# Kernel optimization log

Measured on AMD Instinct MI355X. Metric: run time of the kernel, lower is better.

## Reference

```python
import jax, jax.numpy as jnp
import numpy as np

H_MODEL = 1024
N_HEADS = 16
N_KV_HEADS = 4
HEAD_DIM = 64
SLIDING_WINDOW = 512
B, S = 2, 2048
NEG_INF = -1e9


def rotate_half(x):
    half = x.shape[-1] // 2
    return jnp.concatenate([-x[..., half:], x[..., :half]], axis=-1)


def setup_inputs() -> dict:
    key = jax.random.key(0)
    ks = jax.random.split(key, 8)
    hidden_states = jax.random.normal(ks[0], (B, S, H_MODEL), dtype=jnp.float32)
    # RoPE tables (HF style): cos/sin of shape [1, S, head_dim]
    inv_freq = 1.0 / (10000.0 ** (jnp.arange(0, HEAD_DIM, 2, dtype=jnp.float32) / HEAD_DIM))
    pos = jnp.arange(S, dtype=jnp.float32)
    freqs = jnp.einsum('s,d->sd', pos, inv_freq)            # [S, D/2]
    emb = jnp.concatenate([freqs, freqs], axis=-1)          # [S, D]
    cos = jnp.cos(emb)[None]                                # [1, S, D]
    sin = jnp.sin(emb)[None]
    # additive causal + sliding-window mask [1,1,S,S]
    i = jnp.arange(S)[:, None]
    j = jnp.arange(S)[None, :]
    allowed = (j <= i) & (i - j < SLIDING_WINDOW)
    attention_mask = jnp.where(allowed, 0.0, NEG_INF).astype(jnp.float32)[None, None]
    # projection weights (torch Linear stores [out, in]; y = x @ W.T)
    std = 0.02
    Wq = jax.random.normal(ks[1], (N_HEADS * HEAD_DIM, H_MODEL), dtype=jnp.float32) * std
    Wk = jax.random.normal(ks[2], (N_KV_HEADS * HEAD_DIM, H_MODEL), dtype=jnp.float32) * std
    Wv = jax.random.normal(ks[3], (N_KV_HEADS * HEAD_DIM, H_MODEL), dtype=jnp.float32) * std
    Wo = jax.random.normal(ks[4], (H_MODEL, N_HEADS * HEAD_DIM), dtype=jnp.float32) * std
    return {"hidden_states": hidden_states, "cos": cos, "sin": sin,
            "attention_mask": attention_mask, "Wq": Wq, "Wk": Wk, "Wv": Wv, "Wo": Wo}


def reference(hidden_states, cos, sin, attention_mask, Wq, Wk, Wv, Wo):
    b, s, _ = hidden_states.shape
    G = N_HEADS // N_KV_HEADS
    scaling = HEAD_DIM ** -0.5
    # QKV projections -> [B, H, S, D]
    q = jnp.einsum('bsh,oh->bso', hidden_states, Wq).reshape(b, s, N_HEADS, HEAD_DIM).transpose(0, 2, 1, 3)
    k = jnp.einsum('bsh,oh->bso', hidden_states, Wk).reshape(b, s, N_KV_HEADS, HEAD_DIM).transpose(0, 2, 1, 3)
    v = jnp.einsum('bsh,oh->bso', hidden_states, Wv).reshape(b, s, N_KV_HEADS, HEAD_DIM).transpose(0, 2, 1, 3)
    # RoPE (cos/sin broadcast over head dim via unsqueeze(1))
    c = cos[:, None, :, :]
    sn = sin[:, None, :, :]
    q = q * c + rotate_half(q) * sn
    k = k * c + rotate_half(k) * sn
    # GQA eager attention: group query heads over kv heads
    qg = q.reshape(b, N_KV_HEADS, G, s, HEAD_DIM)
    scores = jnp.einsum('bkgqd,bkpd->bkgqp', qg, k) * scaling  # [B,Hkv,G,S,S]
    scores = scores + attention_mask[:, :, None, :, :]
    probs = jax.nn.softmax(scores.astype(jnp.float32), axis=-1).astype(q.dtype)
    out = jnp.einsum('bkgqp,bkpd->bkgqd', probs, v)            # [B,Hkv,G,S,D]
    out = out.reshape(b, N_HEADS, s, HEAD_DIM).transpose(0, 2, 1, 3).reshape(b, s, N_HEADS * HEAD_DIM)
    return jnp.einsum('bso,ho->bsh', out, Wo)
```

## Files before the change

kernel.cpp:

```cpp
#include <hip/hip_runtime.h>
#include <hip/hip_bf16.h>

#define S_LEN 2048
#define NH 16
#define NKV 4
#define HD 64
#define WIN 512
#define BATCH 2

typedef __bf16 bf16_8 __attribute__((ext_vector_type(8)));
typedef float f32x4 __attribute__((ext_vector_type(4)));

__device__ inline bf16_8 cvt8(f32x4 a, f32x4 b) {
    bf16_8 r;
    r[0] = (__bf16)a[0]; r[1] = (__bf16)a[1]; r[2] = (__bf16)a[2]; r[3] = (__bf16)a[3];
    r[4] = (__bf16)b[0]; r[5] = (__bf16)b[1]; r[6] = (__bf16)b[2]; r[7] = (__bf16)b[3];
    return r;
}


__global__ __launch_bounds__(256) void cvt_pack(
    const float* __restrict__ hs, const float* __restrict__ Wq,
    const float* __restrict__ Wk, const float* __restrict__ Wv,
    const float* __restrict__ Wo,
    __bf16* __restrict__ hsp, __bf16* __restrict__ Wqp,
    __bf16* __restrict__ Wkp, __bf16* __restrict__ Wvp,
    __bf16* __restrict__ Wop)
{
    int i = blockIdx.x * 256 + threadIdx.x;
    const float* S; __bf16* P;
    if (i < 524288)      { S = hs; P = hsp; }
    else if (i < 655360) { S = Wq; P = Wqp; i -= 524288; }
    else if (i < 688128) { S = Wk; P = Wkp; i -= 655360; }
    else if (i < 720896) { S = Wv; P = Wvp; i -= 688128; }
    else                 { S = Wo; P = Wop; i -= 720896; }
    const int n = i >> 7;
    const int k = (i & 127) << 3;
    const f32x4 a = *(const f32x4*)(S + (size_t)n * 1024 + k);
    const f32x4 b = *(const f32x4*)(S + (size_t)n * 1024 + k + 4);
    const size_t dst = ((size_t)((n >> 4) * 32 + (k >> 5)) << 9)
                     + ((size_t)((n & 15) | (((k >> 3) & 3) << 4)) << 3);
    *(bf16_8*)(P + dst) = cvt8(a, b);
}

__device__ __forceinline__ void gemm_stream(
    const __bf16* __restrict__ Aq, const __bf16* __restrict__ Bq,
    f32x4 acc[2][4])
{
    const f32x4 fzero = {0.f, 0.f, 0.f, 0.f};
#pragma unroll
    for (int i = 0; i < 2; ++i)
#pragma unroll
        for (int nt = 0; nt < 4; ++nt) acc[i][nt] = fzero;

    bf16_8 b0[4], b1[4];
#pragma unroll
    for (int nt = 0; nt < 4; ++nt) {
        b0[nt] = *(const bf16_8*)(Bq + nt * 16384);
        b1[nt] = *(const bf16_8*)(Bq + nt * 16384 + 512);
    }

    for (int it = 0; it < 16; ++it) {
        bf16_8 a0[2], a1[2];
#pragma unroll
        for (int i = 0; i < 2; ++i) {
            a0[i] = *(const bf16_8*)(Aq + (size_t)(i * 32 + it * 2) * 512);
            a1[i] = *(const bf16_8*)(Aq + (size_t)(i * 32 + it * 2 + 1) * 512);
        }
        bf16_8 nb0[4], nb1[4];
        const bool pf = it < 15;
        if (pf) {
#pragma unroll
            for (int nt = 0; nt < 4; ++nt) {
                nb0[nt] = *(const bf16_8*)(Bq + nt * 16384 + (it + 1) * 1024);
                nb1[nt] = *(const bf16_8*)(Bq + nt * 16384 + (it + 1) * 1024 + 512);
            }
        }
#pragma unroll
        for (int i = 0; i < 2; ++i)
#pragma unroll
            for (int nt = 0; nt < 4; ++nt)
                acc[i][nt] = __builtin_amdgcn_mfma_f32_16x16x32_bf16(a0[i], b0[nt], acc[i][nt], 0, 0, 0);
#pragma unroll
        for (int i = 0; i < 2; ++i)
#pragma unroll
            for (int nt = 0; nt < 4; ++nt)
                acc[i][nt] = __builtin_amdgcn_mfma_f32_16x16x32_bf16(a1[i], b1[nt], acc[i][nt], 0, 0, 0);
        if (pf) {
#pragma unroll
            for (int nt = 0; nt < 4; ++nt) { b0[nt] = nb0[nt]; b1[nt] = nb1[nt]; }
        }
    }
}

__global__ __launch_bounds__(256, 4) void gemm_qkv(
    const __bf16* __restrict__ Apk,
    const __bf16* __restrict__ Wqp,
    const __bf16* __restrict__ Wkp,
    const __bf16* __restrict__ Wvp,
    __bf16* __restrict__ Qp,
    __bf16* __restrict__ Kf,
    __bf16* __restrict__ Vf,
    const float* __restrict__ cosb,
    const float* __restrict__ sinb)
{
    __shared__ __align__(16) __bf16 smem[9216];

    const int tid  = threadIdx.x;
    const int wave = tid >> 6;
    const int lane = tid & 63;
    const int wm   = wave & 1;
    const int wn   = wave >> 1;
    const int fm   = lane & 15;

    const int bx   = blockIdx.x;
    const int row0 = bx * 64;
    const int by   = blockIdx.y;

    const __bf16* Bp; int colb; int mode;
    if (by < 8)       { Bp = Wqp; colb = by * 128;        mode = 0; }
    else if (by < 10) { Bp = Wkp; colb = (by - 8) * 128;  mode = 1; }
    else              { Bp = Wvp; colb = (by - 10) * 128; mode = 2; }
    const int col0 = colb;

    const __bf16* Bq = Bp + (size_t)((colb + wn * 64) >> 4) * 16384 + (lane << 3);
    const __bf16* Aq = Apk + ((size_t)(bx * 4 + wm * 2) * 32) * 512 + (lane << 3);
    f32x4 acc[2][4];
    gemm_stream(Aq, Bq, acc);

    const int drow = (lane >> 4) << 2;
    const int cq   = col0 + wn * 64;
    const int bb   = row0 >> 11;
    const int sk0  = row0 & (S_LEN - 1);

    if (mode == 0) {
        const int lp = drow | ((fm >> 3) << 4);
#pragma unroll
        for (int i = 0; i < 2; ++i) {
            const size_t t1 = (size_t)(bx * 4 + wm * 2 + i) * 32 + (cq >> 5);
#pragma unroll
            for (int r = 0; r < 4; ++r) {
                const int row = row0 + wm * 32 + i * 16 + drow + r;
                const int s   = row & (S_LEN - 1);
#pragma unroll
                for (int nt = 0; nt < 2; ++nt) {
                    const int d = nt * 16 + fm;
                    const float c1 = cosb[s * HD + d];
                    const float s1 = sinb[s * HD + d];
                    const float c2 = cosb[s * HD + d + 32];
                    const float s2 = sinb[s * HD + d + 32];
                    const float x1 = acc[i][nt][r];
                    const float x2 = acc[i][nt + 2][r];
                    const size_t o = ((size_t)(lp + r + (nt * 2 << 4)) << 3) + (fm & 7);
                    Qp[(t1 << 9) + o]       = (__bf16)(x1 * c1 - x2 * s1);
                    Qp[((t1 + 1) << 9) + o] = (__bf16)(x2 * c2 + x1 * s2);
                }
            }
        }
    } else if (mode == 1) {
        __bf16* T = smem;
#pragma unroll
        for (int i = 0; i < 2; ++i) {
#pragma unroll
            for (int r = 0; r < 4; ++r) {
                const int kl = wm * 32 + i * 16 + drow + r;
                const int s  = sk0 + kl;
#pragma unroll
                for (int nt = 0; nt < 2; ++nt) {
                    const int d = nt * 16 + fm;
                    const float c1 = cosb[s * HD + d];
                    const float s1 = sinb[s * HD + d];
                    const float c2 = cosb[s * HD + d + 32];
                    const float s2 = sinb[s * HD + d + 32];
                    const float x1 = acc[i][nt][r];
                    const float x2 = acc[i][nt + 2][r];
                    T[kl * 136 + wn * 64 + d]      = (__bf16)(x1 * c1 - x2 * s1);
                    T[kl * 136 + wn * 64 + d + 32] = (__bf16)(x2 * c2 + x1 * s2);
                }
            }
        }
        __syncthreads();
#pragma unroll
        for (int c = 0; c < 4; ++c) {
            const int tile = c * 4 + wave;
            const int hh  = tile >> 3;
            const int kt4 = (tile >> 1) & 3;
            const int dd  = tile & 1;
            const int key = kt4 * 16 + fm;
            const int dl  = dd * 32 + ((lane >> 4) << 3);
            const bf16_8 v = *(const bf16_8*)&T[key * 136 + hh * 64 + dl];
            const int khg = (col0 + hh * 64) >> 6;
            const int ktg = (sk0 >> 4) + kt4;
            *(bf16_8*)&Kf[(size_t)(bb * NKV + khg) * 131072 + (size_t)(ktg * 2 + dd) * 512 + lane * 8] = v;
        }
    } else {
        __bf16* T2 = smem;
#pragma unroll
        for (int i = 0; i < 2; ++i)
#pragma unroll
            for (int r = 0; r < 4; ++r)
#pragma unroll
                for (int nt = 0; nt < 4; ++nt)
                    T2[(wn * 64 + nt * 16 + fm) * 72 + wm * 32 + i * 16 + drow + r] =
                        (__bf16)acc[i][nt][r];
        __syncthreads();
#pragma unroll
        for (int c = 0; c < 4; ++c) {
            const int tile = c * 4 + wave;
            const int hh  = tile >> 3;
            const int dd4 = (tile >> 1) & 3;
            const int ks  = tile & 1;
            const int dl  = dd4 * 16 + fm;
            const int key = ks * 32 + ((lane >> 4) << 3);
            const bf16_8 v = *(const bf16_8*)&T2[(hh * 64 + dl) * 72 + key];
            const int khg = (col0 + hh * 64) >> 6;
            const int kvg = (sk0 >> 5) + ks;
            *(bf16_8*)&Vf[(size_t)(bb * NKV + khg) * 131072 + (size_t)(dd4 * 64 + kvg) * 512 + lane * 8] = v;
        }
    }
}

__global__ __launch_bounds__(256, 4) void gemm_o(
    const __bf16* __restrict__ Apk,
    const __bf16* __restrict__ Bp,
    float* __restrict__ C)
{
    const int tid  = threadIdx.x;
    const int wave = tid >> 6;
    const int lane = tid & 63;
    const int wm   = wave & 1;
    const int wn   = wave >> 1;

    const int bx   = blockIdx.x;
    const int row0 = bx * 64;
    const int colb = blockIdx.y * 128;

    const __bf16* Bq = Bp + (size_t)((colb + wn * 64) >> 4) * 16384 + (lane << 3);
    const __bf16* Aq = Apk + ((size_t)(bx * 4 + wm * 2) * 32) * 512 + (lane << 3);
    f32x4 acc[2][4];
    gemm_stream(Aq, Bq, acc);

    const int fm = lane & 15;
    const int drow = (lane >> 4) << 2;
#pragma unroll
    for (int i = 0; i < 2; ++i)
#pragma unroll
        for (int r = 0; r < 4; ++r) {
            const int row = row0 + wm * 32 + i * 16 + drow + r;
#pragma unroll
            for (int nt = 0; nt < 4; ++nt)
                C[(size_t)row * 1024 + colb + wn * 64 + nt * 16 + fm] = acc[i][nt][r];
        }
}

__global__ __launch_bounds__(256) void attn_pk(const __bf16* __restrict__ Qp,
                                               const __bf16* __restrict__ Kf,
                                               const __bf16* __restrict__ Vf,
                                               __bf16* __restrict__ Op)
{
    __shared__ __align__(16) __bf16 Ps[4][16][72];

    const int tid  = threadIdx.x;
    const int wave = tid >> 6;
    const int lane = tid & 63;

    const int bid0 = blockIdx.x;
    const int bid  = (bid0 & 7) * 128 + (bid0 >> 3);

    const int qt = bid & (S_LEN / 64 - 1);
    const int h  = (bid >> 5) & (NH - 1);
    const int b  = bid >> 9;
    const int kh = h >> 2;

    const int q0 = qt * 64;
    const int qw = q0 + wave * 16;

    const int fm = lane & 15;

    const size_t qtile = ((size_t)((b * S_LEN + qw) >> 4) * 32 + h * 2) << 9;
    const bf16_8 qf0 = *(const bf16_8*)&Qp[qtile + (lane << 3)];
    const bf16_8 qf1 = *(const bf16_8*)&Qp[qtile + 512 + (lane << 3)];

    const __bf16* Kfb = Kf + (size_t)(b * NKV + kh) * 131072 + lane * 8;
    const __bf16* Vfb = Vf + (size_t)(b * NKV + kh) * 131072 + lane * 8;

    const f32x4 fzero = {0.f, 0.f, 0.f, 0.f};
    f32x4 oacc[4];
    float l[4];
#pragma unroll
    for (int nt = 0; nt < 4; ++nt) oacc[nt] = fzero;
#pragma unroll
    for (int r = 0; r < 4; ++r) l[r] = 0.f;

    const int qbase = qw + ((lane >> 4) << 2);
    const int fj = (lane >> 4) << 3;

    const int lo  = (qw >= WIN) ? ((qw - WIN + 1) & ~63) : 0;
    const int hi  = (qw + 15) & ~63;
    const int nit = ((hi - lo) >> 6) + 1;

    for (int it = 0; it < nit; ++it) {
        const int kb = lo + (it << 6);

        f32x4 sc[4];
        const int ktb = kb >> 4;
#pragma unroll
        for (int t4 = 0; t4 < 4; ++t4) {
            const bf16_8 k0 = *(const bf16_8*)(Kfb + (size_t)((ktb + t4) * 2) * 512);
            const bf16_8 k1 = *(const bf16_8*)(Kfb + (size_t)((ktb + t4) * 2 + 1) * 512);
            f32x4 s = fzero;
            s = __builtin_amdgcn_mfma_f32_16x16x32_bf16(qf0, k0, s, 0, 0, 0);
            s = __builtin_amdgcn_mfma_f32_16x16x32_bf16(qf1, k1, s, 0, 0, 0);
            sc[t4] = s;
        }

#pragma unroll
        for (int t4 = 0; t4 < 4; ++t4) {
            const int ki = kb + t4 * 16 + fm;
#pragma unroll
            for (int r = 0; r < 4; ++r) {
                const int qr = qbase + r;
                const float e = __expf(sc[t4][r] * 0.125f);
                const float p = (ki <= qr && qr - ki < WIN) ? e : 0.f;
                l[r] += p;
                Ps[wave][((lane >> 4) << 2) + r][t4 * 16 + fm] = (__bf16)p;
            }
        }

        const bf16_8 pf0 = *(const bf16_8*)&Ps[wave][fm][fj];
        const bf16_8 pf1 = *(const bf16_8*)&Ps[wave][fm][32 + fj];

        const int kvb = kb >> 5;
#pragma unroll
        for (int nt = 0; nt < 4; ++nt) {
            const bf16_8 v0 = *(const bf16_8*)(Vfb + (size_t)(nt * 64 + kvb) * 512);
            const bf16_8 v1 = *(const bf16_8*)(Vfb + (size_t)(nt * 64 + kvb + 1) * 512);
            oacc[nt] = __builtin_amdgcn_mfma_f32_16x16x32_bf16(pf0, v0, oacc[nt], 0, 0, 0);
            oacc[nt] = __builtin_amdgcn_mfma_f32_16x16x32_bf16(pf1, v1, oacc[nt], 0, 0, 0);
        }
    }

#pragma unroll
    for (int off = 8; off > 0; off >>= 1)
#pragma unroll
        for (int r = 0; r < 4; ++r)
            l[r] += __shfl_xor(l[r], off, 64);

    const int drow = (lane >> 4) << 2;
    float inv[4];
#pragma unroll
    for (int r = 0; r < 4; ++r) inv[r] = 1.0f / l[r];

    const size_t rt = (size_t)((b * S_LEN + qw) >> 4) * 32;
#pragma unroll
    for (int nt = 0; nt < 4; ++nt) {
        const size_t t = rt + h * 2 + (nt >> 1);
        const int lp0  = drow | (((nt * 2 + (fm >> 3)) & 3) << 4);
        const int e    = fm & 7;
#pragma unroll
        for (int r = 0; r < 4; ++r)
            Op[(t << 9) + ((size_t)(lp0 + r) << 3) + e] = (__bf16)(oacc[nt][r] * inv[r]);
    }
}

extern "C" void kernel_launch(void* const* d_in, const int* in_sizes, int n_in,
                              void* d_out, int out_size, void* d_ws, size_t ws_size,
                              hipStream_t stream)
{
    const float* hs   = (const float*)d_in[0];
    const float* cosb = (const float*)d_in[1];
    const float* sinb = (const float*)d_in[2];
    const float* Wq = (const float*)d_in[4];
    const float* Wk = (const float*)d_in[5];
    const float* Wv = (const float*)d_in[6];
    const float* Wo = (const float*)d_in[7];

    const int M = BATCH * S_LEN;

    __bf16* hsp = (__bf16*)d_ws;
    __bf16* Wqp = hsp + (size_t)M * 1024;
    __bf16* Wkp = Wqp + 1024 * 1024;
    __bf16* Wvp = Wkp + 256 * 1024;
    __bf16* Wop = Wvp + 256 * 1024;
    __bf16* Qpb = Wop + 1024 * 1024;
    __bf16* Kfb = Qpb + (size_t)M * 1024;
    __bf16* Vfb = Kfb + (size_t)8 * 131072;
    __bf16* Opb = Vfb + (size_t)8 * 131072;

    dim3 blk(256);
    cvt_pack<<<3328, blk, 0, stream>>>(hs, Wq, Wk, Wv, Wo,
                                       hsp, Wqp, Wkp, Wvp, Wop);

    gemm_qkv<<<dim3(64, 12), blk, 0, stream>>>(hsp, Wqp, Wkp, Wvp,
                                               Qpb, Kfb, Vfb, cosb, sinb);

    attn_pk<<<BATCH * NH * (S_LEN / 64), blk, 0, stream>>>(Qpb, Kfb, Vfb, Opb);

    gemm_o<<<dim3(64, 8), blk, 0, stream>>>(Opb, Wop, (float*)d_out);
}
```

Before: 165.3 us.

## Stage GEMM tiles through double-buffered LDS using direct global-to-LDS loads

Replaces the register-streaming GEMM core with a shared 64x128 tile routine. Each wave loads a slice of the A and B tiles into a double-buffered LDS area using global_load_lds, so data is shared across waves instead of every wave fetching its own B and A fragments from global memory. This cuts redundant global traffic and overlaps the next stage's loads with the current MFMAs. In exchange it adds LDS use (48KB per block), a barrier every K step, and drops the occupancy hint in launch bounds.

```diff
diff --git a/kernel.cpp b/kernel.cpp
--- a/kernel.cpp
+++ b/kernel.cpp
@@ -16,6 +16,12 @@
     r[0] = (__bf16)a[0]; r[1] = (__bf16)a[1]; r[2] = (__bf16)a[2]; r[3] = (__bf16)a[3];
     r[4] = (__bf16)b[0]; r[5] = (__bf16)b[1]; r[6] = (__bf16)b[2]; r[7] = (__bf16)b[3];
     return r;
+}
+
+typedef __attribute__((address_space(1))) const unsigned int guint;
+typedef __attribute__((address_space(3))) unsigned int luint;
+__device__ __forceinline__ void gload16(const void* g, void* l) {
+    __builtin_amdgcn_global_load_lds((guint*)g, (luint*)l, 16, 0, 0);
 }
 
 
@@ -43,57 +49,74 @@
     *(bf16_8*)(P + dst) = cvt8(a, b);
 }
 
-__device__ __forceinline__ void gemm_stream(
-    const __bf16* __restrict__ Aq, const __bf16* __restrict__ Bq,
-    f32x4 acc[2][4])
-{
+__device__ __forceinline__ void gemm64x128(
+    const __bf16* __restrict__ Apk,
+    const __bf16* __restrict__ Bp,
+    int bx, int colb,
+    __bf16* __restrict__ smem,
+    int tid, f32x4 acc[2][4])
+{
+    const int wave = tid >> 6;
+    const int lane = tid & 63;
+    const int wm   = wave & 1;
+    const int wn   = wave >> 1;
+    const int lofs = lane << 3;
     const f32x4 fzero = {0.f, 0.f, 0.f, 0.f};
 #pragma unroll
     for (int i = 0; i < 2; ++i)
 #pragma unroll
         for (int nt = 0; nt < 4; ++nt) acc[i][nt] = fzero;
 
-    bf16_8 b0[4], b1[4];
-#pragma unroll
-    for (int nt = 0; nt < 4; ++nt) {
-        b0[nt] = *(const bf16_8*)(Bq + nt * 16384);
-        b1[nt] = *(const bf16_8*)(Bq + nt * 16384 + 512);
+    __bf16* As = smem;
+    __bf16* Bs = smem + 8192;
+
+    const __bf16* aSrc  = Apk + ((size_t)(bx * 4 + wave) * 32) * 512 + lofs;
+    const __bf16* bSrc0 = Bp + ((size_t)((colb >> 4) + wave * 2) * 32) * 512 + lofs;
+    const __bf16* bSrc1 = Bp + ((size_t)((colb >> 4) + wave * 2 + 1) * 32) * 512 + lofs;
+
+#define STAGE(buf, it) do {                                            \
+        const int ko = (it) * 2;                                       \
+        __bf16* ad = As + (buf) * 4096 + wave * 1024;                  \
+        gload16(aSrc + (size_t)ko * 512,       ad);                    \
+        gload16(aSrc + (size_t)(ko + 1) * 512, ad + 512);              \
+        __bf16* bd = Bs + (buf) * 8192 + wave * 2048;                  \
+        gload16(bSrc0 + (size_t)ko * 512,       bd);                   \
+        gload16(bSrc0 + (size_t)(ko + 1) * 512, bd + 512);             \
+        gload16(bSrc1 + (size_t)ko * 512,       bd + 1024);            \
+        gload16(bSrc1 + (size_t)(ko + 1) * 512, bd + 1536);            \
+    } while (0)
+
+    STAGE(0, 0);
+    __syncthreads();
+
+#pragma unroll 2
+    for (int it = 0; it < 16; ++it) {
+        const int cur = it & 1;
+        if (it < 15) STAGE(cur ^ 1, it + 1);
+
+        const __bf16* Ab = As + cur * 4096;
+        const __bf16* Bb = Bs + cur * 8192;
+#pragma unroll
+        for (int ks = 0; ks < 2; ++ks) {
+            bf16_8 af[2], bf[4];
+#pragma unroll
+            for (int i = 0; i < 2; ++i)
+                af[i] = *(const bf16_8*)(Ab + ((wm * 2 + i) * 2 + ks) * 512 + lofs);
+#pragma unroll
+            for (int nt = 0; nt < 4; ++nt)
+                bf[nt] = *(const bf16_8*)(Bb + ((wn * 4 + nt) * 2 + ks) * 512 + lofs);
+#pragma unroll
+            for (int i = 0; i < 2; ++i)
+#pragma unroll
+                for (int nt = 0; nt < 4; ++nt)
+                    acc[i][nt] = __builtin_amdgcn_mfma_f32_16x16x32_bf16(af[i], bf[nt], acc[i][nt], 0, 0, 0);
+        }
+        __syncthreads();
     }
-
-    for (int it = 0; it < 16; ++it) {
-        bf16_8 a0[2], a1[2];
-#pragma unroll
-        for (int i = 0; i < 2; ++i) {
-            a0[i] = *(const bf16_8*)(Aq + (size_t)(i * 32 + it * 2) * 512);
-            a1[i] = *(const bf16_8*)(Aq + (size_t)(i * 32 + it * 2 + 1) * 512);
-        }
-        bf16_8 nb0[4], nb1[4];
-        const bool pf = it < 15;
-        if (pf) {
-#pragma unroll
-            for (int nt = 0; nt < 4; ++nt) {
-                nb0[nt] = *(const bf16_8*)(Bq + nt * 16384 + (it + 1) * 1024);
-                nb1[nt] = *(const bf16_8*)(Bq + nt * 16384 + (it + 1) * 1024 + 512);
-            }
-        }
-#pragma unroll
-        for (int i = 0; i < 2; ++i)
-#pragma unroll
-            for (int nt = 0; nt < 4; ++nt)
-                acc[i][nt] = __builtin_amdgcn_mfma_f32_16x16x32_bf16(a0[i], b0[nt], acc[i][nt], 0, 0, 0);
-#pragma unroll
-        for (int i = 0; i < 2; ++i)
-#pragma unroll
-            for (int nt = 0; nt < 4; ++nt)
-                acc[i][nt] = __builtin_amdgcn_mfma_f32_16x16x32_bf16(a1[i], b1[nt], acc[i][nt], 0, 0, 0);
-        if (pf) {
-#pragma unroll
-            for (int nt = 0; nt < 4; ++nt) { b0[nt] = nb0[nt]; b1[nt] = nb1[nt]; }
-        }
-    }
-}
-
-__global__ __launch_bounds__(256, 4) void gemm_qkv(
+#undef STAGE
+}
+
+__global__ __launch_bounds__(256) void gemm_qkv(
     const __bf16* __restrict__ Apk,
     const __bf16* __restrict__ Wqp,
     const __bf16* __restrict__ Wkp,
@@ -104,7 +127,7 @@
     const float* __restrict__ cosb,
     const float* __restrict__ sinb)
 {
-    __shared__ __align__(16) __bf16 smem[9216];
+    __shared__ __align__(16) __bf16 smem[24576];
 
     const int tid  = threadIdx.x;
     const int wave = tid >> 6;
@@ -123,10 +146,8 @@
     else              { Bp = Wvp; colb = (by - 10) * 128; mode = 2; }
     const int col0 = colb;
 
-    const __bf16* Bq = Bp + (size_t)((colb + wn * 64) >> 4) * 16384 + (lane << 3);
-    const __bf16* Aq = Apk + ((size_t)(bx * 4 + wm * 2) * 32) * 512 + (lane << 3);
     f32x4 acc[2][4];
-    gemm_stream(Aq, Bq, acc);
+    gemm64x128(Apk, Bp, bx, colb, smem, tid, acc);
 
     const int drow = (lane >> 4) << 2;
     const int cq   = col0 + wn * 64;
@@ -220,11 +241,13 @@
     }
 }
 
-__global__ __launch_bounds__(256, 4) void gemm_o(
+__global__ __launch_bounds__(256) void gemm_o(
     const __bf16* __restrict__ Apk,
     const __bf16* __restrict__ Bp,
     float* __restrict__ C)
 {
+    __shared__ __align__(16) __bf16 smem[24576];
+
     const int tid  = threadIdx.x;
     const int wave = tid >> 6;
     const int lane = tid & 63;
@@ -235,10 +258,8 @@
     const int row0 = bx * 64;
     const int colb = blockIdx.y * 128;
 
-    const __bf16* Bq = Bp + (size_t)((colb + wn * 64) >> 4) * 16384 + (lane << 3);
-    const __bf16* Aq = Apk + ((size_t)(bx * 4 + wm * 2) * 32) * 512 + (lane << 3);
     f32x4 acc[2][4];
-    gemm_stream(Aq, Bq, acc);
+    gemm64x128(Apk, Bp, bx, colb, smem, tid, acc);
 
     const int fm = lane & 15;
     const int drow = (lane >> 4) << 2;
```

New measurement: 157.0 us. 1.05x faster.
